# Optimization experiments

Hardware: AMD Instinct MI355X
Metric: run time of the kernel (lower is better)

The kernel has to match this reference:

```python
import jax, jax.numpy as jnp
import numpy as np

EPS = 1e-5  # BatchNorm eps (torch default)

def setup_inputs() -> dict:
    key = jax.random.key(0)
    ks = jax.random.split(key, 12)
    B, C, H, W = 4, 256, 64, 64
    IC = 128  # inter_channels = C // 2
    s = 1.0 / np.sqrt(C)
    si = 1.0 / np.sqrt(IC)
    return {
        "x": jax.random.normal(ks[0], (B, C, H, W), jnp.float32),
        "y": jax.random.normal(ks[1], (B, C, H, W), jnp.float32),
        "g_w": jax.random.normal(ks[2], (IC, C), jnp.float32) * s,
        "g_b": jax.random.normal(ks[3], (IC,), jnp.float32) * 0.01,
        "dx_w": jax.random.normal(ks[4], (IC, C), jnp.float32) * s,
        "dx_b": jax.random.normal(ks[5], (IC,), jnp.float32) * 0.01,
        "dy_w": jax.random.normal(ks[6], (IC, C), jnp.float32) * s,
        "dy_b": jax.random.normal(ks[7], (IC,), jnp.float32) * 0.01,
        "w_w": jax.random.normal(ks[8], (C, IC), jnp.float32) * si,
        "w_b": jax.random.normal(ks[9], (C,), jnp.float32) * 0.01,
        "bn_gamma": jax.random.normal(ks[10], (C,), jnp.float32),
        "bn_beta": jax.random.normal(ks[11], (C,), jnp.float32) * 0.01,
    }

def _conv1x1(t, w, b):
    # t: [B,C,H,W], w: [O,C], b: [O] -> [B,O,H,W]
    return jnp.einsum('bchw,oc->bohw', t, w) + b[None, :, None, None]

def reference(x, y, g_w, g_b, dx_w, dx_b, dy_w, dy_b, w_w, w_b, bn_gamma, bn_beta):
    B, C, H, W = x.shape
    IC = g_w.shape[0]
    N = H * W
    g_y = _conv1x1(y, g_w, g_b).reshape(B, IC, N).transpose(0, 2, 1)      # [B,N,IC]
    theta_x = _conv1x1(x, dx_w, dx_b).reshape(B, IC, N).transpose(0, 2, 1)  # [B,N,IC]
    phi_y = _conv1x1(y, dy_w, dy_b).reshape(B, IC, N)                      # [B,IC,N]
    f = jnp.einsum('bnc,bcm->bnm', theta_x, phi_y)                         # [B,N,N]
    f_div_C = jax.nn.softmax(f, axis=-1)
    y2 = jnp.einsum('bnm,bmc->bnc', f_div_C, g_y)                          # [B,N,IC]
    y2 = y2.transpose(0, 2, 1).reshape(B, IC, H, W)
    wy = _conv1x1(y2, w_w, w_b)                                            # [B,C,H,W]
    # BatchNorm2d in training mode: batch stats over (B,H,W) per channel
    mean = jnp.mean(wy, axis=(0, 2, 3), keepdims=True)
    var = jnp.var(wy, axis=(0, 2, 3), keepdims=True)
    wy_bn = (wy - mean) / jnp.sqrt(var + EPS)
    wy_bn = wy_bn * bn_gamma[None, :, None, None] + bn_beta[None, :, None, None]
    return wy_bn + x
```

## Files before the change

### kernel.cpp

```cpp
#include <hip/hip_runtime.h>
#include <hip/hip_bf16.h>
#include <math.h>

typedef unsigned short ushort_t;
typedef __attribute__((ext_vector_type(8))) short     short8;
typedef __attribute__((ext_vector_type(8))) _Float16  half8;
typedef __attribute__((ext_vector_type(8))) unsigned short ushort8;
typedef __attribute__((ext_vector_type(4))) float     float4v;
typedef __attribute__((ext_vector_type(16))) float    floatx16;

__device__ __forceinline__ float b2f(ushort_t u) {
    return __uint_as_float(((unsigned)u) << 16);
}
__device__ __forceinline__ ushort_t f2b(float f) {
    unsigned i = __float_as_uint(f);
    return (ushort_t)((i + 0x7FFFu + ((i >> 16) & 1u)) >> 16);
}
__device__ __forceinline__ void split2(float v, ushort_t& h, ushort_t& l) {
    h = f2b(v);
    l = f2b(v - b2f(h));
}
__device__ __forceinline__ void glds16(const ushort_t* g, ushort_t* l) {
    __builtin_amdgcn_global_load_lds((const __attribute__((address_space(1))) void*)g,
                                     (__attribute__((address_space(3))) void*)l, 16, 0, 0);
}
__device__ __forceinline__ unsigned int pack2bf(float lo, float hi) {
    unsigned int r;
    asm("v_cvt_pk_bf16_f32 %0, %1, %2" : "=v"(r) : "v"(lo), "v"(hi));
    return r;
}
__device__ __forceinline__ void pl32swap(unsigned int& a, unsigned int& b) {
    asm("v_permlane32_swap_b32 %0, %1" : "+v"(a), "+v"(b));
}

#define WTFH_OFF   0
#define WTFL_OFF   196608
#define WWBH_OFF   393216
#define WWBL_OFF   458752
#define BIAS_OFF   524288
#define PROJF_OFF  1048576
#define GT_OFF     9437184
#define OPART_OFF  13631488
#define WY_OFF     1048576
#define PART_OFF   9437184

__global__ void prep_k(const float* __restrict__ dx_w, const float* __restrict__ dy_w,
                       const float* __restrict__ g_w,  const float* __restrict__ dx_b,
                       const float* __restrict__ dy_b, const float* __restrict__ g_b,
                       const float* __restrict__ w_w,
                       ushort_t* __restrict__ wtfh, ushort_t* __restrict__ wtfl,
                       ushort_t* __restrict__ wwbh, ushort_t* __restrict__ wwbl,
                       float* __restrict__ bias) {
    int idx = blockIdx.x * 256 + threadIdx.x;
    int j = idx & 7, lane = (idx >> 3) & 63, kk = (idx >> 9) & 7, ot = idx >> 12;
    int o = ot * 16 + (lane & 15);
    int c = kk * 32 + ((lane >> 4) * 8) + j;
    float v;
    if (o < 128)      v = dx_w[o * 256 + c];
    else if (o < 256) v = dy_w[(o - 128) * 256 + c];
    else              v = g_w[(o - 256) * 256 + c];
    ushort_t h, l;
    split2(v, h, l);
    wtfh[idx] = h; wtfl[idx] = l;
    if (idx < 32768) {
        split2(w_w[idx], h, l);
        wwbh[idx] = h; wwbl[idx] = l;
    }
    if (idx < 384) {
        bias[idx] = (idx < 128) ? dx_b[idx]
                  : (idx < 256) ? dy_b[idx - 128]
                                : g_b[idx - 256];
    }
}

#define XTS 258
__global__ __launch_bounds__(256) void proj_k(const float* __restrict__ x,
                                              const float* __restrict__ y,
                                              const ushort_t* __restrict__ wtfh,
                                              const ushort_t* __restrict__ wtfl,
                                              const float* __restrict__ bias,
                                              ushort_t* __restrict__ projf,
                                              ushort_t* __restrict__ gT) {
    __shared__ ushort_t xT[2][32 * XTS];
    int b = blockIdx.y, n0 = blockIdx.x * 32;
    int tid = threadIdx.x;
    int w = tid >> 6, lane = tid & 63;
    int mrow = lane & 15, quad = lane >> 4, koff = quad * 8;
    int half = w & 1, sect = w >> 1;
    int arow = half * 16 + mrow;

    for (int s = 0; s < 2; s++) {
        if (s) __syncthreads();
        const float* src = s ? y : x;
        #pragma unroll
        for (int i = 0; i < 4; i++) {
            int ch = tid + i * 256;
            int c = ch >> 2, off = (ch & 3) * 8;
            const float* p = src + (size_t)(b * 256 + c) * 4096 + n0 + off;
            float4v v0 = *(const float4v*)p;
            float4v v1 = *(const float4v*)(p + 4);
            #pragma unroll
            for (int jj = 0; jj < 4; jj++) {
                ushort_t h, l;
                split2(v0[jj], h, l);
                xT[0][(off + jj) * XTS + c] = h;
                xT[1][(off + jj) * XTS + c] = l;
                split2(v1[jj], h, l);
                xT[0][(off + 4 + jj) * XTS + c] = h;
                xT[1][(off + 4 + jj) * XTS + c] = l;
            }
        }
        __syncthreads();

        short8 fh[8], fl[8];
        #pragma unroll
        for (int kk = 0; kk < 8; kk++) {
            fh[kk] = *(const short8*)&xT[0][arow * XTS + kk * 32 + koff];
            fl[kk] = *(const short8*)&xT[1][arow * XTS + kk * 32 + koff];
        }

        int ot0 = s ? (8 + sect * 8) : (sect * 4);
        int ot1 = s ? (ot0 + 8) : (ot0 + 4);
        for (int ot = ot0; ot < ot1; ot++) {
            float4v acc = {0.f, 0.f, 0.f, 0.f};
            #pragma unroll
            for (int kk = 0; kk < 8; kk++) {
                short8 bh = *(const short8*)(wtfh + (size_t)((ot * 8 + kk) * 64 + lane) * 8);
                short8 bl = *(const short8*)(wtfl + (size_t)((ot * 8 + kk) * 64 + lane) * 8);
                acc = __builtin_amdgcn_mfma_f32_16x16x32_bf16(fh[kk], bh, acc, 0, 0, 0);
                acc = __builtin_amdgcn_mfma_f32_16x16x32_bf16(fh[kk], bl, acc, 0, 0, 0);
                acc = __builtin_amdgcn_mfma_f32_16x16x32_bf16(fl[kk], bh, acc, 0, 0, 0);
            }
            int o = ot * 16 + mrow;
            float bo = bias[o];
            #pragma unroll
            for (int r = 0; r < 4; r++) {
                int n = n0 + half * 16 + quad * 4 + r;
                float v = acc[r] + bo;
                if (ot < 16) {
                    _Float16 hf = (_Float16)v;
                    projf[(size_t)(b * 4096 + n) * 256 + o] = *(ushort_t*)&hf;
                } else {
                    gT[(size_t)(b * 128 + (o - 256)) * 4096 + n] = f2b(v);
                }
            }
        }
    }
}

template<int KVB>
__global__ __launch_bounds__(256, (KVB == 32 ? 4 : 2))
void flash_k(const ushort_t* __restrict__ projf,
             const ushort_t* __restrict__ gT,
             float* __restrict__ opart,
             float* __restrict__ oml,
             int kqlog) {
    constexpr int NT2 = KVB / 32;
    constexpr int NCH = KVB / 4;
    constexpr int NPT = NCH / 4;
    __shared__ __align__(16) ushort_t KsF[2][KVB * 128];
    __shared__ __align__(16) ushort_t VsF[2][KVB * 128];

    int L = blockIdx.x;
    int xcd = L & 7, t = L >> 3;
    int c, j;
    if (kqlog >= 2)      { c = (t >> 5) * 8 + xcd; j = t & 31; }
    else if (kqlog == 1) { c = xcd;                j = t; }
    else                 { c = xcd & 3;            j = t + ((xcd >> 2) << 4); }
    int b  = c >> kqlog;
    int kq = c & ((1 << kqlog) - 1);
    int q0 = j * 128;
    int iters = (4096 >> kqlog) / KVB;
    int kt0 = kq * iters;
    int tid = threadIdx.x, w = tid >> 6, lane = tid & 63;
    int ln = lane & 31, hh = lane >> 5;

    const ushort_t* kSrc[NPT];
    const ushort_t* vSrc[NPT];
    {
        int kb0 = kt0 * KVB;
        #pragma unroll
        for (int i = 0; i < NPT; i++) {
            int cc = w + i * 4;
            int t2 = cc >> 3, kk = cc & 7;
            kSrc[i] = projf + (size_t)(b * 4096 + kb0 + t2 * 32 + ln) * 256 + 128 + kk * 16 + hh * 8;
            int it = cc / (2 * NT2), g = cc % (2 * NT2);
            vSrc[i] = gT + (size_t)(b * 128 + it * 32 + ln) * 4096 + kb0 + g * 16 + hh * 8;
        }
    }

    half8 qf[8];
    {
        const ushort_t* qp = projf + (size_t)(b * 4096 + q0 + w * 32 + ln) * 256 + hh * 8;
        #pragma unroll
        for (int kk = 0; kk < 8; kk++)
            qf[kk] = *(const half8*)(qp + kk * 16);
    }

    floatx16 oacc[4];
    #pragma unroll
    for (int it = 0; it < 4; it++)
        #pragma unroll
        for (int jj = 0; jj < 16; jj++) oacc[it][jj] = 0.f;
    float lacc[NT2];
    #pragma unroll
    for (int t2 = 0; t2 < NT2; t2++) lacc[t2] = 0.f;

    #pragma unroll
    for (int i = 0; i < NPT; i++) {
        int cc = w + i * 4;
        glds16(kSrc[i], &KsF[0][cc * 512]);
        glds16(vSrc[i], &VsF[0][cc * 512]);
        kSrc[i] += (size_t)KVB * 256;
        vSrc[i] += KVB;
    }

    for (int kt = kt0; kt < kt0 + iters; kt++) {
        int cur = (kt - kt0) & 1;
        __syncthreads();
        if (kt + 1 < kt0 + iters) {
            #pragma unroll
            for (int i = 0; i < NPT; i++) {
                int cc = w + i * 4;
                glds16(kSrc[i], &KsF[1 - cur][cc * 512]);
                glds16(vSrc[i], &VsF[1 - cur][cc * 512]);
                kSrc[i] += (size_t)KVB * 256;
                vSrc[i] += KVB;
            }
        }

        floatx16 sacc[NT2];
        #pragma unroll
        for (int t2 = 0; t2 < NT2; t2++)
            #pragma unroll
            for (int jj = 0; jj < 16; jj++) sacc[t2][jj] = 0.f;
        __builtin_amdgcn_s_setprio(1);
        #pragma unroll
        for (int kk = 0; kk < 8; kk++) {
            #pragma unroll
            for (int t2 = 0; t2 < NT2; t2++) {
                half8 ah = *(const half8*)&KsF[cur][((t2 * 8 + kk) * 64 + lane) * 8];
                sacc[t2] = __builtin_amdgcn_mfma_f32_32x32x16_f16(ah, qf[kk], sacc[t2], 0, 0, 0);
            }
        }
        __builtin_amdgcn_s_setprio(0);

        short8 fr[2 * NT2];
        #pragma unroll
        for (int t2 = 0; t2 < NT2; t2++) {
            float ps[16];
            #pragma unroll
            for (int r = 0; r < 16; r++)
                ps[r] = __builtin_exp2f(fmaf(sacc[t2][r], 1.44269504f, -92.332481f));
            lacc[t2] += ((((ps[0] + ps[1]) + (ps[2] + ps[3]))
                        + ((ps[4] + ps[5]) + (ps[6] + ps[7])))
                       + (((ps[8] + ps[9]) + (ps[10] + ps[11]))
                        + ((ps[12] + ps[13]) + (ps[14] + ps[15]))));
            unsigned int pw[8];
            #pragma unroll
            for (int c2 = 0; c2 < 8; c2++) pw[c2] = pack2bf(ps[2 * c2], ps[2 * c2 + 1]);
            pl32swap(pw[0], pw[2]);
            pl32swap(pw[1], pw[3]);
            pl32swap(pw[4], pw[6]);
            pl32swap(pw[5], pw[7]);
            union { unsigned int u[4]; short8 s8; } fA, fB;
            fA.u[0] = pw[0]; fA.u[1] = pw[1]; fA.u[2] = pw[2]; fA.u[3] = pw[3];
            fB.u[0] = pw[4]; fB.u[1] = pw[5]; fB.u[2] = pw[6]; fB.u[3] = pw[7];
            fr[t2 * 2]     = fA.s8;
            fr[t2 * 2 + 1] = fB.s8;
        }

        __builtin_amdgcn_s_setprio(1);
        #pragma unroll
        for (int it = 0; it < 4; it++) {
            #pragma unroll
            for (int kg = 0; kg < 2 * NT2; kg++) {
                short8 vv = *(const short8*)&VsF[cur][((it * 2 * NT2 + kg) * 64 + lane) * 8];
                oacc[it] = __builtin_amdgcn_mfma_f32_32x32x16_bf16(fr[kg], vv, oacc[it], 0, 0, 0);
            }
        }
        __builtin_amdgcn_s_setprio(0);
    }

    {
        int rowBase = b * 4096 + q0 + w * 32 + hh * 4;
        #pragma unroll
        for (int it = 0; it < 4; it++)
            #pragma unroll
            for (int r = 0; r < 16; r++) {
                int qrow = rowBase + (r & 3) + 8 * (r >> 2);
                opart[((size_t)kq * 16384 + qrow) * 128 + it * 32 + ln] = oacc[it][r];
            }
    }
    float lsum = lacc[0];
    #pragma unroll
    for (int t2 = 1; t2 < NT2; t2++) lsum += lacc[t2];
    lsum += __shfl_xor(lsum, 32, 64);
    if (lane < 32)
        oml[kq * 16384 + b * 4096 + q0 + w * 32 + lane] = lsum;
}

template<int KQ>
__global__ __launch_bounds__(256) void wy_k(const float* __restrict__ opart,
                                            const float* __restrict__ oml,
                                            const ushort_t* __restrict__ wwbh,
                                            const ushort_t* __restrict__ wwbl,
                                            const float* __restrict__ w_b,
                                            ushort_t* __restrict__ wy,
                                            float* __restrict__ part) {
    int b = blockIdx.y, n0 = blockIdx.x * 32;
    int tid = threadIdx.x, w = tid >> 6, lane = tid & 63;
    int mrow = lane & 15, quad = lane >> 4, koff = quad * 8;
    int half = w & 1, sect = w >> 1;
    int Rn = b * 4096 + n0 + half * 16 + mrow;

    float L = 0.f;
    #pragma unroll
    for (int kq = 0; kq < KQ; kq++) L += oml[kq * 16384 + Rn];
    float invL = 1.f / L;

    short8 bfh[4], bfl[4];
    #pragma unroll
    for (int kk = 0; kk < 4; kk++) {
        float a[8];
        #pragma unroll
        for (int j = 0; j < 8; j++) a[j] = 0.f;
        #pragma unroll
        for (int kq = 0; kq < KQ; kq++) {
            const float* p = opart + ((size_t)kq * 16384 + Rn) * 128 + kk * 32 + koff;
            float4v v0 = *(const float4v*)p;
            float4v v1 = *(const float4v*)(p + 4);
            #pragma unroll
            for (int j = 0; j < 4; j++) { a[j] += v0[j]; a[4 + j] += v1[j]; }
        }
        #pragma unroll
        for (int j = 0; j < 8; j++) {
            ushort_t h, l;
            split2(a[j] * invL, h, l);
            bfh[kk][j] = (short)h; bfl[kk][j] = (short)l;
        }
    }

    int coln = n0 + half * 16 + mrow;
    int pcol = (blockIdx.x * 4 + b) * 2 + half;
    for (int cot = sect * 8; cot < sect * 8 + 8; cot++) {
        float4v acc = {0.f, 0.f, 0.f, 0.f};
        #pragma unroll
        for (int kk = 0; kk < 4; kk++) {
            size_t woff = (size_t)(cot * 16 + mrow) * 128 + kk * 32 + koff;
            short8 ah = *(const short8*)(wwbh + woff);
            short8 al = *(const short8*)(wwbl + woff);
            acc = __builtin_amdgcn_mfma_f32_16x16x32_bf16(ah, bfh[kk], acc, 0, 0, 0);
            acc = __builtin_amdgcn_mfma_f32_16x16x32_bf16(ah, bfl[kk], acc, 0, 0, 0);
            acc = __builtin_amdgcn_mfma_f32_16x16x32_bf16(al, bfh[kk], acc, 0, 0, 0);
        }
        float s1v[4], s2v[4];
        #pragma unroll
        for (int r = 0; r < 4; r++) {
            int co = cot * 16 + quad * 4 + r;
            ushort_t bv = f2b(acc[r] + w_b[co]);
            wy[(size_t)(b * 256 + co) * 4096 + coln] = bv;
            float vb = b2f(bv);
            s1v[r] = vb; s2v[r] = vb * vb;
        }
        #pragma unroll
        for (int d = 1; d < 16; d <<= 1) {
            #pragma unroll
            for (int r = 0; r < 4; r++) {
                s1v[r] += __shfl_xor(s1v[r], d, 64);
                s2v[r] += __shfl_xor(s2v[r], d, 64);
            }
        }
        if (mrow == 0) {
            #pragma unroll
            for (int r = 0; r < 4; r++) {
                int co = cot * 16 + quad * 4 + r;
                part[co * 1024 + pcol]          = s1v[r];
                part[262144 + co * 1024 + pcol] = s2v[r];
            }
        }
    }
}

__global__ __launch_bounds__(256) void bn_k(const ushort_t* __restrict__ wy,
                                            const float* __restrict__ x,
                                            const float* __restrict__ gamma,
                                            const float* __restrict__ beta,
                                            const float* __restrict__ part,
                                            float* __restrict__ out) {
    __shared__ float red[8];
    __shared__ float sc[2];
    int tid = threadIdx.x, w = tid >> 6, lane = tid & 63;
    int idx = (blockIdx.x * 256 + tid) * 8;
    int c = (idx >> 12) & 255;

    float4v p1 = *(const float4v*)(part + c * 1024 + tid * 4);
    float4v p2 = *(const float4v*)(part + 262144 + c * 1024 + tid * 4);
    float s  = (p1[0] + p1[1]) + (p1[2] + p1[3]);
    float s2 = (p2[0] + p2[1]) + (p2[2] + p2[3]);
    #pragma unroll
    for (int d = 1; d < 64; d <<= 1) { s += __shfl_xor(s, d, 64); s2 += __shfl_xor(s2, d, 64); }
    if (lane == 0) { red[w] = s; red[4 + w] = s2; }
    __syncthreads();
    if (tid == 0) {
        float S  = (red[0] + red[1]) + (red[2] + red[3]);
        float S2 = (red[4] + red[5]) + (red[6] + red[7]);
        const float inv_cnt = 1.f / 16384.f;
        float mean = S * inv_cnt;
        float var  = S2 * inv_cnt - mean * mean;
        float inv  = rsqrtf(var + 1e-5f);
        float scale = gamma[c] * inv;
        sc[0] = scale;
        sc[1] = beta[c] - mean * scale;
    }
    __syncthreads();
    float scale = sc[0], shift = sc[1];

    ushort8 wv = *(const ushort8*)(wy + idx);
    float4v x0 = *(const float4v*)(x + idx);
    float4v x1 = *(const float4v*)(x + idx + 4);
    float4v o0, o1;
    #pragma unroll
    for (int j = 0; j < 4; j++) {
        o0[j] = b2f(wv[j]) * scale + shift + x0[j];
        o1[j] = b2f(wv[4 + j]) * scale + shift + x1[j];
    }
    *(float4v*)(out + idx) = o0;
    *(float4v*)(out + idx + 4) = o1;
}

extern "C" void kernel_launch(void* const* d_in, const int* in_sizes, int n_in,
                              void* d_out, int out_size, void* d_ws, size_t ws_size,
                              hipStream_t stream) {
    const float* x    = (const float*)d_in[0];
    const float* y    = (const float*)d_in[1];
    const float* g_w  = (const float*)d_in[2];
    const float* g_b  = (const float*)d_in[3];
    const float* dx_w = (const float*)d_in[4];
    const float* dx_b = (const float*)d_in[5];
    const float* dy_w = (const float*)d_in[6];
    const float* dy_b = (const float*)d_in[7];
    const float* w_w  = (const float*)d_in[8];
    const float* w_b  = (const float*)d_in[9];
    const float* bn_g = (const float*)d_in[10];
    const float* bn_b = (const float*)d_in[11];

    char* ws = (char*)d_ws;
    ushort_t* wtfh  = (ushort_t*)(ws + WTFH_OFF);
    ushort_t* wtfl  = (ushort_t*)(ws + WTFL_OFF);
    ushort_t* wwbh  = (ushort_t*)(ws + WWBH_OFF);
    ushort_t* wwbl  = (ushort_t*)(ws + WWBL_OFF);
    float*    bias  = (float*)(ws + BIAS_OFF);
    ushort_t* projf = (ushort_t*)(ws + PROJF_OFF);
    ushort_t* gT    = (ushort_t*)(ws + GT_OFF);
    float*    opart = (float*)(ws + OPART_OFF);
    ushort_t* wy    = (ushort_t*)(ws + WY_OFF);
    float*    part  = (float*)(ws + PART_OFF);
    float*    out   = (float*)d_out;

    int kqlog;
    if      (ws_size >= 13631488u + 4u * (8388608u + 65536u)) kqlog = 2;
    else if (ws_size >= 13631488u + 2u * (8388608u + 65536u)) kqlog = 1;
    else                                                      kqlog = 0;
    int KQ = 1 << kqlog;
    float* oml = (float*)(ws + OPART_OFF + (size_t)KQ * 8388608u);

    prep_k<<<384, 256, 0, stream>>>(dx_w, dy_w, g_w, dx_b, dy_b, g_b, w_w,
                                    wtfh, wtfl, wwbh, wwbl, bias);
    proj_k<<<dim3(128, 4), 256, 0, stream>>>(x, y, wtfh, wtfl, bias, projf, gT);
    flash_k<64><<<dim3(128 << kqlog), 256, 0, stream>>>(projf, gT, opart, oml, kqlog);
    if (KQ == 4)
        wy_k<4><<<dim3(128, 4), 256, 0, stream>>>(opart, oml, wwbh, wwbl, w_b, wy, part);
    else if (KQ == 2)
        wy_k<2><<<dim3(128, 4), 256, 0, stream>>>(opart, oml, wwbh, wwbl, w_b, wy, part);
    else
        wy_k<1><<<dim3(128, 4), 256, 0, stream>>>(opart, oml, wwbh, wwbl, w_b, wy, part);
    bn_k<<<2048, 256, 0, stream>>>(wy, x, bn_g, bn_b, part, out);
}
```

Measured before the change: 214.1 us.

## Split KV tile across wave pairs in flash kernel with 512-thread blocks

The flash attention kernel moves from 4 to 8 waves per block. Each pair of waves shares 32 query rows and splits the 64-key tile in halves, so each wave holds one score accumulator instead of two. The two halves' partial outputs and row sums are combined through shared memory at the end. The aim is more waves in flight and fewer registers per wave to hide latency, at the cost of a cross-wave reduction epilogue and duplicated Q fragment loads.

```diff
diff --git a/kernel.cpp b/kernel.cpp
--- a/kernel.cpp
+++ b/kernel.cpp
@@ -148,18 +148,13 @@
     }
 }
 
-template<int KVB>
-__global__ __launch_bounds__(256, (KVB == 32 ? 4 : 2))
+__global__ __launch_bounds__(512, 4)
 void flash_k(const ushort_t* __restrict__ projf,
              const ushort_t* __restrict__ gT,
              float* __restrict__ opart,
              float* __restrict__ oml,
              int kqlog) {
-    constexpr int NT2 = KVB / 32;
-    constexpr int NCH = KVB / 4;
-    constexpr int NPT = NCH / 4;
-    __shared__ __align__(16) ushort_t KsF[2][KVB * 128];
-    __shared__ __align__(16) ushort_t VsF[2][KVB * 128];
+    __shared__ __align__(16) ushort_t smem[2][16384];
 
     int L = blockIdx.x;
     int xcd = L & 7, t = L >> 3;
@@ -170,28 +165,28 @@
     int b  = c >> kqlog;
     int kq = c & ((1 << kqlog) - 1);
     int q0 = j * 128;
-    int iters = (4096 >> kqlog) / KVB;
+    int iters = (4096 >> kqlog) / 64;
     int kt0 = kq * iters;
     int tid = threadIdx.x, w = tid >> 6, lane = tid & 63;
     int ln = lane & 31, hh = lane >> 5;
-
-    const ushort_t* kSrc[NPT];
-    const ushort_t* vSrc[NPT];
+    int qw = w >> 1, s = w & 1;
+
+    const ushort_t* kSrc[2];
+    const ushort_t* vSrc[2];
     {
-        int kb0 = kt0 * KVB;
-        #pragma unroll
-        for (int i = 0; i < NPT; i++) {
-            int cc = w + i * 4;
-            int t2 = cc >> 3, kk = cc & 7;
-            kSrc[i] = projf + (size_t)(b * 4096 + kb0 + t2 * 32 + ln) * 256 + 128 + kk * 16 + hh * 8;
-            int it = cc / (2 * NT2), g = cc % (2 * NT2);
+        int kb0 = kt0 * 64;
+        #pragma unroll
+        for (int i = 0; i < 2; i++) {
+            int cc = w + i * 8;
+            kSrc[i] = projf + (size_t)(b * 4096 + kb0 + i * 32 + ln) * 256 + 128 + w * 16 + hh * 8;
+            int it = cc >> 2, g = cc & 3;
             vSrc[i] = gT + (size_t)(b * 128 + it * 32 + ln) * 4096 + kb0 + g * 16 + hh * 8;
         }
     }
 
     half8 qf[8];
     {
-        const ushort_t* qp = projf + (size_t)(b * 4096 + q0 + w * 32 + ln) * 256 + hh * 8;
+        const ushort_t* qp = projf + (size_t)(b * 4096 + q0 + qw * 32 + ln) * 256 + hh * 8;
         #pragma unroll
         for (int kk = 0; kk < 8; kk++)
             qf[kk] = *(const half8*)(qp + kk * 16);
@@ -202,17 +197,15 @@
     for (int it = 0; it < 4; it++)
         #pragma unroll
         for (int jj = 0; jj < 16; jj++) oacc[it][jj] = 0.f;
-    float lacc[NT2];
-    #pragma unroll
-    for (int t2 = 0; t2 < NT2; t2++) lacc[t2] = 0.f;
-
-    #pragma unroll
-    for (int i = 0; i < NPT; i++) {
-        int cc = w + i * 4;
-        glds16(kSrc[i], &KsF[0][cc * 512]);
-        glds16(vSrc[i], &VsF[0][cc * 512]);
-        kSrc[i] += (size_t)KVB * 256;
-        vSrc[i] += KVB;
+    float lsum = 0.f;
+
+    #pragma unroll
+    for (int i = 0; i < 2; i++) {
+        int cc = w + i * 8;
+        glds16(kSrc[i], &smem[0][cc * 512]);
+        glds16(vSrc[i], &smem[0][8192 + cc * 512]);
+        kSrc[i] += (size_t)64 * 256;
+        vSrc[i] += 64;
     }
 
     for (int kt = kt0; kt < kt0 + iters; kt++) {
@@ -220,84 +213,94 @@
         __syncthreads();
         if (kt + 1 < kt0 + iters) {
             #pragma unroll
-            for (int i = 0; i < NPT; i++) {
-                int cc = w + i * 4;
-                glds16(kSrc[i], &KsF[1 - cur][cc * 512]);
-                glds16(vSrc[i], &VsF[1 - cur][cc * 512]);
-                kSrc[i] += (size_t)KVB * 256;
-                vSrc[i] += KVB;
-            }
-        }
-
-        floatx16 sacc[NT2];
-        #pragma unroll
-        for (int t2 = 0; t2 < NT2; t2++)
-            #pragma unroll
-            for (int jj = 0; jj < 16; jj++) sacc[t2][jj] = 0.f;
+            for (int i = 0; i < 2; i++) {
+                int cc = w + i * 8;
+                glds16(kSrc[i], &smem[1 - cur][cc * 512]);
+                glds16(vSrc[i], &smem[1 - cur][8192 + cc * 512]);
+                kSrc[i] += (size_t)64 * 256;
+                vSrc[i] += 64;
+            }
+        }
+
+        floatx16 sacc;
+        #pragma unroll
+        for (int jj = 0; jj < 16; jj++) sacc[jj] = 0.f;
         __builtin_amdgcn_s_setprio(1);
         #pragma unroll
         for (int kk = 0; kk < 8; kk++) {
-            #pragma unroll
-            for (int t2 = 0; t2 < NT2; t2++) {
-                half8 ah = *(const half8*)&KsF[cur][((t2 * 8 + kk) * 64 + lane) * 8];
-                sacc[t2] = __builtin_amdgcn_mfma_f32_32x32x16_f16(ah, qf[kk], sacc[t2], 0, 0, 0);
-            }
+            half8 ah = *(const half8*)&smem[cur][((s * 8 + kk) * 64 + lane) * 8];
+            sacc = __builtin_amdgcn_mfma_f32_32x32x16_f16(ah, qf[kk], sacc, 0, 0, 0);
         }
         __builtin_amdgcn_s_setprio(0);
 
-        short8 fr[2 * NT2];
-        #pragma unroll
-        for (int t2 = 0; t2 < NT2; t2++) {
-            float ps[16];
-            #pragma unroll
-            for (int r = 0; r < 16; r++)
-                ps[r] = __builtin_exp2f(fmaf(sacc[t2][r], 1.44269504f, -92.332481f));
-            lacc[t2] += ((((ps[0] + ps[1]) + (ps[2] + ps[3]))
-                        + ((ps[4] + ps[5]) + (ps[6] + ps[7])))
-                       + (((ps[8] + ps[9]) + (ps[10] + ps[11]))
-                        + ((ps[12] + ps[13]) + (ps[14] + ps[15]))));
-            unsigned int pw[8];
-            #pragma unroll
-            for (int c2 = 0; c2 < 8; c2++) pw[c2] = pack2bf(ps[2 * c2], ps[2 * c2 + 1]);
-            pl32swap(pw[0], pw[2]);
-            pl32swap(pw[1], pw[3]);
-            pl32swap(pw[4], pw[6]);
-            pl32swap(pw[5], pw[7]);
-            union { unsigned int u[4]; short8 s8; } fA, fB;
-            fA.u[0] = pw[0]; fA.u[1] = pw[1]; fA.u[2] = pw[2]; fA.u[3] = pw[3];
-            fB.u[0] = pw[4]; fB.u[1] = pw[5]; fB.u[2] = pw[6]; fB.u[3] = pw[7];
-            fr[t2 * 2]     = fA.s8;
-            fr[t2 * 2 + 1] = fB.s8;
-        }
+        float ps[16];
+        #pragma unroll
+        for (int r = 0; r < 16; r++)
+            ps[r] = __builtin_exp2f(fmaf(sacc[r], 1.44269504f, -92.332481f));
+        lsum += ((((ps[0] + ps[1]) + (ps[2] + ps[3]))
+                + ((ps[4] + ps[5]) + (ps[6] + ps[7])))
+               + (((ps[8] + ps[9]) + (ps[10] + ps[11]))
+                + ((ps[12] + ps[13]) + (ps[14] + ps[15]))));
+        unsigned int pw[8];
+        #pragma unroll
+        for (int c2 = 0; c2 < 8; c2++) pw[c2] = pack2bf(ps[2 * c2], ps[2 * c2 + 1]);
+        pl32swap(pw[0], pw[2]);
+        pl32swap(pw[1], pw[3]);
+        pl32swap(pw[4], pw[6]);
+        pl32swap(pw[5], pw[7]);
+        union { unsigned int u[4]; short8 s8; } fA, fB;
+        fA.u[0] = pw[0]; fA.u[1] = pw[1]; fA.u[2] = pw[2]; fA.u[3] = pw[3];
+        fB.u[0] = pw[4]; fB.u[1] = pw[5]; fB.u[2] = pw[6]; fB.u[3] = pw[7];
 
         __builtin_amdgcn_s_setprio(1);
         #pragma unroll
         for (int it = 0; it < 4; it++) {
-            #pragma unroll
-            for (int kg = 0; kg < 2 * NT2; kg++) {
-                short8 vv = *(const short8*)&VsF[cur][((it * 2 * NT2 + kg) * 64 + lane) * 8];
-                oacc[it] = __builtin_amdgcn_mfma_f32_32x32x16_bf16(fr[kg], vv, oacc[it], 0, 0, 0);
-            }
+            short8 v0 = *(const short8*)&smem[cur][8192 + ((it * 4 + s * 2) * 64 + lane) * 8];
+            short8 v1 = *(const short8*)&smem[cur][8192 + ((it * 4 + s * 2 + 1) * 64 + lane) * 8];
+            oacc[it] = __builtin_amdgcn_mfma_f32_32x32x16_bf16(fA.s8, v0, oacc[it], 0, 0, 0);
+            oacc[it] = __builtin_amdgcn_mfma_f32_32x32x16_bf16(fB.s8, v1, oacc[it], 0, 0, 0);
         }
         __builtin_amdgcn_s_setprio(0);
     }
 
-    {
-        int rowBase = b * 4096 + q0 + w * 32 + hh * 4;
-        #pragma unroll
-        for (int it = 0; it < 4; it++)
-            #pragma unroll
-            for (int r = 0; r < 16; r++) {
-                int qrow = rowBase + (r & 3) + 8 * (r >> 2);
-                opart[((size_t)kq * 16384 + qrow) * 128 + it * 32 + ln] = oacc[it][r];
-            }
-    }
-    float lsum = lacc[0];
-    #pragma unroll
-    for (int t2 = 1; t2 < NT2; t2++) lsum += lacc[t2];
-    lsum += __shfl_xor(lsum, 32, 64);
-    if (lane < 32)
-        oml[kq * 16384 + b * 4096 + q0 + w * 32 + lane] = lsum;
+    __syncthreads();
+    float* fs = (float*)smem;
+    #pragma unroll
+    for (int ph = 0; ph < 2; ph++) {
+        if (s == 1) {
+            #pragma unroll
+            for (int i2 = 0; i2 < 2; i2++) {
+                int it = ph * 2 + i2;
+                #pragma unroll
+                for (int r = 0; r < 16; r++) {
+                    int rloc = hh * 4 + (r & 3) + 8 * (r >> 2);
+                    fs[(qw * 32 + rloc) * 64 + i2 * 32 + ln] = oacc[it][r];
+                }
+            }
+            if (ph == 0) fs[8192 + qw * 64 + lane] = lsum;
+        }
+        __syncthreads();
+        if (s == 0) {
+            #pragma unroll
+            for (int i2 = 0; i2 < 2; i2++) {
+                int it = ph * 2 + i2;
+                #pragma unroll
+                for (int r = 0; r < 16; r++) {
+                    int rloc = hh * 4 + (r & 3) + 8 * (r >> 2);
+                    int qrow = b * 4096 + q0 + qw * 32 + rloc;
+                    float o = oacc[it][r] + fs[(qw * 32 + rloc) * 64 + i2 * 32 + ln];
+                    opart[((size_t)kq * 16384 + qrow) * 128 + it * 32 + ln] = o;
+                }
+            }
+            if (ph == 0) {
+                float lt = lsum + fs[8192 + qw * 64 + lane];
+                lt += __shfl_xor(lt, 32, 64);
+                if (lane < 32)
+                    oml[kq * 16384 + b * 4096 + q0 + qw * 32 + lane] = lt;
+            }
+        }
+        __syncthreads();
+    }
 }
 
 template<int KQ>
@@ -468,7 +471,7 @@
     prep_k<<<384, 256, 0, stream>>>(dx_w, dy_w, g_w, dx_b, dy_b, g_b, w_w,
                                     wtfh, wtfl, wwbh, wwbl, bias);
     proj_k<<<dim3(128, 4), 256, 0, stream>>>(x, y, wtfh, wtfl, bias, projf, gT);
-    flash_k<64><<<dim3(128 << kqlog), 256, 0, stream>>>(projf, gT, opart, oml, kqlog);
+    flash_k<<<dim3(128 << kqlog), 512, 0, stream>>>(projf, gT, opart, oml, kqlog);
     if (KQ == 4)
         wy_k<4><<<dim3(128, 4), 256, 0, stream>>>(opart, oml, wwbh, wwbl, w_b, wy, part);
     else if (KQ == 2)
```

New measurement: 223.2 us. 4.3% more time.
